# Optimization experiments

Measured on AMD Instinct MI355X. Metric: run time of the kernel, lower is better.

Reference implementation:

```python
import jax, jax.numpy as jnp
import numpy as np

T, B, D = 256, 64, 1024  # time steps, batch (envs), hidden/input dim


def setup_inputs() -> dict:
    key = jax.random.key(0)
    ks = jax.random.split(key, 8)
    s = 1.0 / np.sqrt(D).astype(np.float32)  # lecun-normal-ish scale
    return {
        "ins": jax.random.normal(ks[0], (T, B, D), jnp.float32),
        "hiddens": jax.random.normal(ks[1], (T, B, D), jnp.float32),
        "dones": jax.random.randint(ks[2], (T, B), 0, 2).astype(bool),
        "init_carry": jax.random.normal(ks[3], (B, D), jnp.float32),
        # concatenated input->hidden weights [D, 3D] for (r, z, n) gates
        "W_i": jax.random.normal(ks[4], (D, 3 * D), jnp.float32) * s,
        # concatenated hidden->hidden weights [D, 3D] for (r, z, n) gates
        "W_h": jax.random.normal(ks[5], (D, 3 * D), jnp.float32) * s,
        # input-side biases (b_ir, b_iz, b_in)
        "b_i": jax.random.normal(ks[6], (3 * D,), jnp.float32) * 0.01,
        # hidden-side bias for the 'n' gate only (flax GRUCell: hn Dense has bias)
        "b_hn": jax.random.normal(ks[7], (D,), jnp.float32) * 0.01,
    }


def reference(ins, hiddens, dones, init_carry, W_i, W_h, b_i, b_hn):
    # Hoist input projections out of the scan (same math as per-step Dense)
    x_proj = jnp.einsum('tbd,de->tbe', ins, W_i) + b_i  # [T, B, 3D]
    xr, xz, xn = jnp.split(x_proj, 3, axis=-1)
    W_hr, W_hz, W_hn = jnp.split(W_h, 3, axis=1)

    def step(h, inp):
        xr_t, xz_t, xn_t, hid_t, done_t = inp
        # reset hidden state where episode terminated
        h = jnp.where(done_t[:, None], hid_t, h)
        r = jax.nn.sigmoid(xr_t + h @ W_hr)
        z = jax.nn.sigmoid(xz_t + h @ W_hz)
        n = jnp.tanh(xn_t + r * (h @ W_hn + b_hn))
        h_new = (1.0 - z) * n + z * h  # flax GRUCell update
        return h_new, h_new  # GRUCell returns (new_carry, new_carry)

    final_carry, ys = jax.lax.scan(step, init_carry, (xr, xz, xn, hiddens, dones))
    return final_carry, ys
```

## Files before the change

### kernel.cpp

```cpp
#include <hip/hip_runtime.h>
#include <hip/hip_bf16.h>
#include <stdint.h>


#define T_STEPS 256
#define NB 64
#define DIM 1024
#define NPH 32

typedef unsigned short u16;
typedef __attribute__((ext_vector_type(8))) short bf16x8;
typedef __attribute__((ext_vector_type(4))) float f32x4;

__device__ __forceinline__ float b2f(u16 u){ union{unsigned i; float f;} v; v.i=((unsigned)u)<<16; return v.f; }
__device__ __forceinline__ u16 f2b(float f){
  union { __hip_bfloat16 h; u16 u; } v; v.h = __float2bfloat16(f); return v.u;
}
__device__ __forceinline__ unsigned pk2(float lo, float hi){
  union { __hip_bfloat162 h; unsigned u; } v;
  v.h = __float22bfloat162_rn(make_float2(lo, hi));
  return v.u;
}
__device__ __forceinline__ float sigf(float x){ return 1.0f/(1.0f+__expf(-x)); }
__device__ __forceinline__ float tanh_f(float x){ float ax=fabsf(x); float e=__expf(-2.0f*ax); float t=(1.0f-e)/(1.0f+e); return copysignf(t,x); }

__device__ __forceinline__ int xcdswz(int raw, int n){
  int xcd = raw & 7, idx = raw >> 3;
  int q = n >> 3, r = n & 7;
  int base = (xcd < r) ? xcd*(q+1) : r*(q+1) + (xcd-r)*q;
  return base + idx;
}

__device__ __forceinline__ void gl_lds16(const u16* g, u16* lbase, int lane){
#if __has_builtin(__builtin_amdgcn_global_load_lds)
  __builtin_amdgcn_global_load_lds(
      (const __attribute__((address_space(1))) unsigned int*)g,
      (__attribute__((address_space(3))) unsigned int*)lbase, 16, 0, 0);
#else
  *(uint4*)(lbase + lane*8) = *(const uint4*)g;
#endif
}

__device__ __forceinline__ void stage16(const void* base, size_t eoff, int isf, u16* dst){
  if (isf){
    const float* f = (const float*)base + eoff;
    f32x4 a0 = *(const f32x4*)f;
    f32x4 a1 = *(const f32x4*)(f+4);
    uint4 w;
    w.x = pk2(a0[0],a0[1]); w.y = pk2(a0[2],a0[3]);
    w.z = pk2(a1[0],a1[1]); w.w = pk2(a1[2],a1[3]);
    *(uint4*)dst = w;
  } else {
    *(uint4*)dst = *(const uint4*)((const u16*)base + eoff);
  }
}

__device__ __forceinline__ int get_mode(const int* d){
  return (!d[0]) ? 0 : ((!d[1]) ? 3 : ((!d[2]) ? 2 : 1));
}
__device__ __forceinline__ int get_done(const void* dn, int mode, int i){
  if (mode == 0) return ((const int*)dn)[i] != 0;
  if (mode == 3) return ((const unsigned*)dn)[i] != 0;
  if (mode == 2) return ((const u16*)dn)[i] != 0;
  return ((const unsigned char*)dn)[i] != 0;
}

__global__ void k_setup0(const void* dones, const void* ins, int* cnt, int* cur, int* dflag){
  int tid = threadIdx.x;
  if (tid < NPH){ cnt[tid]=0; cur[tid]=0; }
  if (tid < 4) dflag[tid]=0;
  __syncthreads();
  const unsigned* di = (const unsigned*)dones;
  int vInt=0, vF32=0, vB16=0;
  for (int i = tid; i < 4096; i += 256){
    unsigned v = di[i];
    if (v > 1u) vInt = 1;
    if (v != 0u && v != 0x3F800000u) vF32 = 1;
    unsigned h0 = v & 0xFFFFu, h1 = v >> 16;
    if ((h0 != 0u && h0 != 0x3F80u) || (h1 != 0u && h1 != 0x3F80u)) vB16 = 1;
  }
  if (vInt) atomicOr(&dflag[0], 1);
  if (vF32) atomicOr(&dflag[1], 1);
  if (vB16) atomicOr(&dflag[2], 1);
  const u16* iu = (const u16*)ins;
  int f = 0;
  for (int i = tid; i < 4096; i += 256){
    u16 u = iu[2*i];
    if (((u >> 7) & 0xFF) >= 160) f = 1;
  }
  if (f) atomicOr(&dflag[3], 1);
}

__global__ void k_assign(const void* dones, const int* dflag, int* s_of, int* cnt){
  __shared__ unsigned char sd[T_STEPS];
  int b = blockIdx.x, t = threadIdx.x;
  int mode = get_mode(dflag);
  sd[t] = (unsigned char)get_done(dones, mode, t*NB + b);
  __syncthreads();
  int tt = t;
  while (tt > 0 && !sd[tt]) --tt;
  int s = t - tt;
  if (s >= NPH) s = NPH-1;
  s_of[t*NB + b] = s;
  atomicAdd(&cnt[s], 1);
}

__global__ void k_scan(const int* cnt, int* basep, int* cur){
  if (threadIdx.x == 0){
    int a = 0;
    for (int i=0;i<NPH;++i){ basep[i]=a; a += cnt[i]; }
    basep[NPH] = a;
  }
  if (threadIdx.x < NPH) cur[threadIdx.x] = 0;
}

__global__ void k_fill(const void* dones, const int* dflag, const int* s_of,
                       const int* basep, int* row_tb, int* row_src){
  int s = blockIdx.x;
  __shared__ int runbase;
  __shared__ int wsum[4];
  int tid = threadIdx.x, lane = tid & 63, wave = tid >> 6;
  int mode = get_mode(dflag);
  if (tid == 0) runbase = basep[s];
  __syncthreads();
  for (int i0 = 0; i0 < T_STEPS*NB; i0 += 256){
    int i = i0 + tid;
    int match = (s_of[i] == s);
    unsigned long long mask = __ballot(match);
    if (lane == 0) wsum[wave] = __popcll(mask);
    __syncthreads();
    int off = runbase;
    for (int w = 0; w < wave; ++w) off += wsum[w];
    int total = wsum[0] + wsum[1] + wsum[2] + wsum[3];
    if (match){
      int pos = off + __popcll(mask & ((1ull << lane) - 1ull));
      row_tb[pos] = i;
      int t = i >> 6, b = i & 63;
      int code;
      if (s > 0) code = (t-1)*NB + b;
      else if (get_done(dones, mode, i)) code = i | 0x40000000;
      else code = b | 0x20000000;
      row_src[pos] = code;
    }
    __syncthreads();
    if (tid == 0) runbase += total;
  }
}

__global__ void k_transpose(const void* __restrict__ W, u16* __restrict__ WT, const int* dflag){
  __shared__ u16 ts[64][65];
  int k0 = blockIdx.x*64, n0 = blockIdx.y*64, tid = threadIdx.x;
  int isf = dflag[3];
  for (int i = tid; i < 4096; i += 256){
    int r=i>>6, c=i&63; int idx=(k0+r)*3072 + n0 + c;
    ts[r][c] = isf ? f2b(((const float*)W)[idx]) : ((const u16*)W)[idx];
  }
  __syncthreads();
  for (int i = tid; i < 4096; i += 256){
    int r=i>>6, c=i&63;
    WT[(n0+r)*DIM + k0 + c] = ts[c][r];
  }
}

__global__ void k_bias(const void* bi, const void* bhn, const int* dflag,
                       u16* bi_b, u16* bhn_b){
  int isf = dflag[3];
  int i = blockIdx.x*256 + threadIdx.x;
  if (i < 3072) bi_b[i] = isf ? f2b(((const float*)bi)[i]) : ((const u16*)bi)[i];
  else { int j=i-3072; bhn_b[j] = isf ? f2b(((const float*)bhn)[j]) : ((const u16*)bhn)[j]; }
}

__device__ __forceinline__ void hsrc(int code, const void* outv, const void* hiddens,
                                     const void* initc, const void** hb, size_t* ho){
  if (code & 0x40000000){ *hb = hiddens; *ho = (size_t)(code & 0x0FFFFFFF)*DIM; }
  else if (code & 0x20000000){ *hb = initc; *ho = (size_t)(code & 0x0FFFFFFF)*DIM; }
  else { *hb = outv; *ho = (size_t)NB*DIM + (size_t)code*DIM; }
}

__global__ __launch_bounds__(256, 2) void k_xproj(
    const void* __restrict__ ins, const u16* __restrict__ WiT,
    const int* __restrict__ dflag, u16* __restrict__ xp)
{
  __shared__ u16 As[2][128*64];
  __shared__ u16 Bs[2][128*64];
  int isf = dflag[3];
  int tid=threadIdx.x, wave=tid>>6, lane=tid&63, quad=lane>>4, l16=lane&15;
  int wm=wave&1, wn=wave>>1;
  int srow = wave*8 + (lane>>3), c8=(lane&7)*8;
  int swzc = c8 ^ ((srow&7)<<3);
  int rsw = (l16&7)<<3;
  int l = xcdswz(blockIdx.x, 3072);
  int tn = l % 24, tm = l / 24;
  f32x4 acc[4][4] = {};
  unsigned aoff[4], boff[4];
  #pragma unroll
  for (int p=0;p<4;++p){
    aoff[p] = (unsigned)(tm*128 + p*32 + srow)*DIM + c8;
    boff[p] = (unsigned)(tn*128 + p*32 + srow)*DIM + swzc;
  }
  #pragma unroll
  for (int p=0;p<4;++p) gl_lds16(WiT + boff[p], &Bs[0][(p*32+wave*8)*64], lane);
  #pragma unroll
  for (int p=0;p<4;++p) stage16(ins, aoff[p], isf, &As[0][(p*32+srow)*64 + swzc]);
  __syncthreads();
  int cur = 0;
  #pragma unroll 1
  for (int ko=64; ko<1024; ko+=64){
    #pragma unroll
    for (int p=0;p<4;++p) gl_lds16(WiT + boff[p] + ko, &Bs[cur^1][(p*32+wave*8)*64], lane);
    f32x4 pr0[4], pr1[4];
    #pragma unroll
    for (int p=0;p<4;++p){
      if (isf){ const float* f=(const float*)ins + aoff[p] + ko; pr0[p]=*(const f32x4*)f; pr1[p]=*(const f32x4*)(f+4); }
      else pr0[p]=*(const f32x4*)((const u16*)ins + aoff[p] + ko);
    }
    #pragma unroll
    for (int kk=0;kk<64;kk+=32){
      int rc = (kk + quad*8) ^ rsw;
      bf16x8 af[4], bfv[4];
      #pragma unroll
      for (int mi=0;mi<4;++mi) af[mi]  = *(const bf16x8*)&As[cur][(wm*64+mi*16+l16)*64 + rc];
      #pragma unroll
      for (int ni=0;ni<4;++ni) bfv[ni] = *(const bf16x8*)&Bs[cur][(wn*64+ni*16+l16)*64 + rc];
      #pragma unroll
      for (int mi=0;mi<4;++mi)
        #pragma unroll
        for (int ni=0;ni<4;++ni)
          acc[mi][ni] = __builtin_amdgcn_mfma_f32_16x16x32_bf16(af[mi],bfv[ni],acc[mi][ni],0,0,0);
    }
    #pragma unroll
    for (int p=0;p<4;++p){
      uint4 w;
      if (isf){ w.x=pk2(pr0[p][0],pr0[p][1]); w.y=pk2(pr0[p][2],pr0[p][3]);
                w.z=pk2(pr1[p][0],pr1[p][1]); w.w=pk2(pr1[p][2],pr1[p][3]); }
      else { union{f32x4 f; uint4 u;} cv; cv.f=pr0[p]; w=cv.u; }
      *(uint4*)&As[cur^1][(p*32+srow)*64 + swzc] = w;
    }
    __syncthreads();
    cur ^= 1;
  }
  #pragma unroll
  for (int kk=0;kk<64;kk+=32){
    int rc = (kk + quad*8) ^ rsw;
    bf16x8 af[4], bfv[4];
    #pragma unroll
    for (int mi=0;mi<4;++mi) af[mi]  = *(const bf16x8*)&As[cur][(wm*64+mi*16+l16)*64 + rc];
    #pragma unroll
    for (int ni=0;ni<4;++ni) bfv[ni] = *(const bf16x8*)&Bs[cur][(wn*64+ni*16+l16)*64 + rc];
    #pragma unroll
    for (int mi=0;mi<4;++mi)
      #pragma unroll
      for (int ni=0;ni<4;++ni)
        acc[mi][ni] = __builtin_amdgcn_mfma_f32_16x16x32_bf16(af[mi],bfv[ni],acc[mi][ni],0,0,0);
  }
  #pragma unroll
  for (int mi=0;mi<4;++mi){
    int row = tm*128 + wm*64 + mi*16 + quad*4;
    #pragma unroll
    for (int ni=0;ni<4;++ni){
      int colB = tn*128 + wn*64 + ni*16 + l16;
      u16* op = xp + (size_t)row*3072 + colB;
      #pragma unroll
      for (int j=0;j<4;++j)
        op[(size_t)j*3072] = f2b(acc[mi][ni][j]);
    }
  }
}

#define FAT_MFMA(BUF, NGRP)                                                    \
        _Pragma("unroll")                                                      \
        for (int kk=0;kk<64;kk+=32){                                           \
          int rc = (kk + quad*8) ^ rsw;                                        \
          bf16x8 af[4];                                                        \
          _Pragma("unroll")                                                    \
          for (int mi=0;mi<4;++mi)                                             \
            af[mi] = *(const bf16x8*)&As[BUF][(wm*64+mi*16+l16)*64 + rc];      \
          _Pragma("unroll")                                                    \
          for (int g=0;g<3;++g){                                               \
            int grp = (g==2) ? (NGRP) : g;                                     \
            _Pragma("unroll")                                                  \
            for (int ni=0;ni<2;++ni){                                          \
              bf16x8 bfr = *(const bf16x8*)&Bs[BUF][(g*64+wn*32+ni*16+l16)*64 + rc]; \
              _Pragma("unroll")                                                \
              for (int mi=0;mi<4;++mi)                                         \
                acc[grp][mi][ni] = __builtin_amdgcn_mfma_f32_16x16x32_bf16(af[mi],bfr,acc[grp][mi][ni],0,0,0); \
            }                                                                  \
          }                                                                    \
        }

#define FAT_PANEL(BASEARR, OFFARR, WTP, NGRP)                                  \
    {                                                                          \
      __syncthreads();                                                         \
      _Pragma("unroll")                                                        \
      for (int p=0;p<6;++p)                                                    \
        gl_lds16(WTP + boffB[p], &Bs[0][(p*32+wave*8)*64], lane);              \
      _Pragma("unroll")                                                        \
      for (int p=0;p<4;++p)                                                    \
        stage16(BASEARR[p], OFFARR[p], isf, &As[0][(p*32+srow)*64 + swzc]);    \
      __syncthreads();                                                         \
      int cur = 0;                                                             \
      _Pragma("unroll 1")                                                      \
      for (int ko=64; ko<1024; ko+=64){                                        \
        _Pragma("unroll")                                                      \
        for (int p=0;p<6;++p)                                                  \
          gl_lds16(WTP + boffB[p] + ko, &Bs[cur^1][(p*32+wave*8)*64], lane);   \
        f32x4 pr0[4], pr1[4];                                                  \
        _Pragma("unroll")                                                      \
        for (int p=0;p<4;++p){                                                 \
          if (isf){ const float* f=(const float*)BASEARR[p]+OFFARR[p]+ko;      \
            pr0[p]=*(const f32x4*)f; pr1[p]=*(const f32x4*)(f+4); }            \
          else pr0[p]=*(const f32x4*)((const u16*)BASEARR[p]+OFFARR[p]+ko);    \
        }                                                                      \
        FAT_MFMA(cur, NGRP)                                                    \
        _Pragma("unroll")                                                      \
        for (int p=0;p<4;++p){                                                 \
          uint4 w;                                                             \
          if (isf){ w.x=pk2(pr0[p][0],pr0[p][1]); w.y=pk2(pr0[p][2],pr0[p][3]);\
                    w.z=pk2(pr1[p][0],pr1[p][1]); w.w=pk2(pr1[p][2],pr1[p][3]);}\
          else { union{f32x4 f; uint4 u;} cv; cv.f=pr0[p]; w=cv.u; }           \
          *(uint4*)&As[cur^1][(p*32+srow)*64 + swzc] = w;                      \
        }                                                                      \
        __syncthreads();                                                       \
        cur ^= 1;                                                              \
      }                                                                        \
      FAT_MFMA(cur, NGRP)                                                      \
    }

template<bool HOIST>
__global__ __launch_bounds__(256, 2) void phase_fat(
    int s, const int* __restrict__ pcnt, const int* __restrict__ pbase,
    const int* __restrict__ row_tb, const int* __restrict__ row_src,
    const void* __restrict__ ins, const void* __restrict__ hiddens,
    const void* __restrict__ initc, const u16* __restrict__ WiT,
    const u16* __restrict__ WhT, const u16* __restrict__ bi_b,
    const u16* __restrict__ bhn_b, const int* __restrict__ dflag,
    const u16* __restrict__ xp, void* __restrict__ outv)
{
  int count = pcnt[s];
  if (count <= 0) return;
  int isf = dflag[3];
  int base = pbase[s];
  int mtiles = (count + 127) >> 7;
  int ntot = mtiles << 4;
  __shared__ u16 As[2][128*64];
  __shared__ u16 Bs[2][192*64];
  int tid=threadIdx.x, wave=tid>>6, lane=tid&63, quad=lane>>4, l16=lane&15;
  int wm=wave&1, wn=wave>>1;
  int srow = wave*8 + (lane>>3), c8=(lane&7)*8;
  int swzc = c8 ^ ((srow&7)<<3);
  int rsw = (l16&7)<<3;
  constexpr int NG = HOIST ? 3 : 4;

  for (int raw = blockIdx.x; raw < ntot; raw += gridDim.x){
    int tile = xcdswz(raw, ntot);
    int tm = tile >> 4, dblk = tile & 15, d0 = dblk*64;
    unsigned xoff[4], hoff[4];
    const void* hbv[4];
    const void* xbv[4];
    #pragma unroll
    for (int p=0;p<4;++p){
      int lr = tm*128 + p*32 + srow;
      int idx = base + ((lr < count) ? lr : 0);
      int tb = row_tb[idx], code = row_src[idx];
      xoff[p] = (unsigned)tb*DIM + c8;
      xbv[p] = ins;
      size_t ho; const void* hb;
      hsrc(code, outv, hiddens, initc, &hb, &ho);
      hbv[p] = hb; hoff[p] = (unsigned)ho + c8;
    }
    int boffB[6];
    #pragma unroll
    for (int p=0;p<6;++p)
      boffB[p] = ((p>>1)*DIM + d0 + (p&1)*32 + srow)*DIM + swzc;
    f32x4 acc[NG][4][2] = {};

    if constexpr (!HOIST){
      FAT_PANEL(xbv, xoff, WiT, 2)
    }
    FAT_PANEL(hbv, hoff, WhT, (NG-1))

    int col0 = d0 + wn*32;
    float brv[2], bzv[2], bnv[2], bhv[2];
    #pragma unroll
    for (int ni=0;ni<2;++ni){
      int c = col0 + ni*16 + l16;
      brv[ni]=b2f(bi_b[c]); bzv[ni]=b2f(bi_b[1024+c]);
      bnv[ni]=b2f(bi_b[2048+c]); bhv[ni]=b2f(bhn_b[c]);
    }
    #pragma unroll
    for (int mi=0;mi<4;++mi){
      int lrow0 = tm*128 + wm*64 + mi*16 + quad*4;
      #pragma unroll
      for (int j=0;j<4;++j){
        int lrow = lrow0 + j;
        if (lrow >= count) continue;
        int idx = base + lrow;
        int tb = row_tb[idx], code = row_src[idx];
        size_t ho; const void* hb;
        hsrc(code, outv, hiddens, initc, &hb, &ho);
        #pragma unroll
        for (int ni=0;ni<2;++ni){
          int c = col0 + ni*16 + l16;
          float hpv = isf ? ((const float*)hb)[ho + c] : b2f(((const u16*)hb)[ho + c]);
          float xr = 0.f, xz = 0.f, xn = 0.f;
          if constexpr (HOIST){
            const u16* xrow = xp + (size_t)tb*3072 + c;
            xr = b2f(xrow[0]); xz = b2f(xrow[1024]); xn = b2f(xrow[2048]);
          }
          float r = sigf(brv[ni] + xr + acc[0][mi][ni][j]);
          float z = sigf(bzv[ni] + xz + acc[1][mi][ni][j]);
          float nx = HOIST ? xn : acc[2][mi][ni][j];
          float n = tanh_f(bnv[ni] + nx + r*(acc[NG-1][mi][ni][j] + bhv[ni]));
          float hnew = (1.0f - z)*n + z*hpv;
          size_t yo = (size_t)NB*DIM + (size_t)tb*DIM + c;
          if (isf) ((float*)outv)[yo] = hnew;
          else     ((u16*)outv)[yo] = f2b(hnew);
        }
      }
    }
  }
}

#define THIN_MFMA(BUF, NGRP)                                                   \
      _Pragma("unroll")                                                        \
      for (int kk=0;kk<64;kk+=32){                                             \
        int rc = (kk + quad*8) ^ rsw;                                          \
        bf16x8 af = *(const bf16x8*)&As[BUF][(wave*16+l16)*64 + rc];           \
        _Pragma("unroll")                                                      \
        for (int g=0;g<3;++g){                                                 \
          bf16x8 bfr = *(const bf16x8*)&Bs[BUF][(g*16+l16)*64 + rc];           \
          int grp = (g==2) ? (NGRP) : g;                                       \
          acc[grp] = __builtin_amdgcn_mfma_f32_16x16x32_bf16(af,bfr,acc[grp],0,0,0); \
        }                                                                      \
      }

#define THIN_PANEL(BASEARR, OFFARR, WTP, NGRP)                                 \
    {                                                                          \
      __syncthreads();                                                         \
      gl_lds16(WTP + boffA, &Bs[0][(wave*8)*64], lane);                        \
      if (wave < 2) gl_lds16(WTP + boffC, &Bs[0][(32+wave*8)*64], lane);       \
      stage16(BASEARR[0], OFFARR[0], isf, &As[0][srow*64 + swzc]);             \
      stage16(BASEARR[1], OFFARR[1], isf, &As[0][(32+srow)*64 + swzc]);        \
      __syncthreads();                                                         \
      int cur = 0;                                                             \
      _Pragma("unroll 1")                                                      \
      for (int ko=64; ko<1024; ko+=64){                                        \
        gl_lds16(WTP + boffA + ko, &Bs[cur^1][(wave*8)*64], lane);             \
        if (wave < 2) gl_lds16(WTP + boffC + ko, &Bs[cur^1][(32+wave*8)*64], lane); \
        f32x4 pr0[2], pr1[2];                                                  \
        _Pragma("unroll")                                                      \
        for (int p=0;p<2;++p){                                                 \
          if (isf){ const float* f=(const float*)BASEARR[p]+OFFARR[p]+ko;      \
            pr0[p]=*(const f32x4*)f; pr1[p]=*(const f32x4*)(f+4); }            \
          else pr0[p]=*(const f32x4*)((const u16*)BASEARR[p]+OFFARR[p]+ko);    \
        }                                                                      \
        THIN_MFMA(cur, NGRP)                                                   \
        _Pragma("unroll")                                                      \
        for (int p=0;p<2;++p){                                                 \
          uint4 w;                                                             \
          if (isf){ w.x=pk2(pr0[p][0],pr0[p][1]); w.y=pk2(pr0[p][2],pr0[p][3]);\
                    w.z=pk2(pr1[p][0],pr1[p][1]); w.w=pk2(pr1[p][2],pr1[p][3]);}\
          else { union{f32x4 f; uint4 u;} cv; cv.f=pr0[p]; w=cv.u; }           \
          *(uint4*)&As[cur^1][(p*32+srow)*64 + swzc] = w;                      \
        }                                                                      \
        __syncthreads();                                                       \
        cur ^= 1;                                                              \
      }                                                                        \
      THIN_MFMA(cur, NGRP)                                                     \
    }

template<bool HOIST>
__global__ __launch_bounds__(256, 4) void phase_thin(
    int s, const int* __restrict__ pcnt, const int* __restrict__ pbase,
    const int* __restrict__ row_tb, const int* __restrict__ row_src,
    const void* __restrict__ ins, const void* __restrict__ hiddens,
    const void* __restrict__ initc, const u16* __restrict__ WiT,
    const u16* __restrict__ WhT, const u16* __restrict__ bi_b,
    const u16* __restrict__ bhn_b, const int* __restrict__ dflag,
    const u16* __restrict__ xp, void* __restrict__ outv)
{
  int count = pcnt[s];
  if (count <= 0) return;
  int isf = dflag[3];
  int base = pbase[s];
  int mtiles = (count + 63) >> 6;
  int ntot = mtiles << 6;
  __shared__ u16 As[2][64*64];
  __shared__ u16 Bs[2][48*64];
  int tid=threadIdx.x, wave=tid>>6, lane=tid&63, quad=lane>>4, l16=lane&15;
  int srow = wave*8 + (lane>>3), c8=(lane&7)*8;
  int swzc = c8 ^ ((srow&7)<<3);
  int rsw = (l16&7)<<3;
  constexpr int NG = HOIST ? 3 : 4;

  for (int tile = blockIdx.x; tile < ntot; tile += gridDim.x){
    int tm = tile >> 6, dblk = tile & 63, d0 = dblk*16;
    unsigned xoff[2], hoff[2];
    const void* hbv[2];
    const void* xbv[2];
    #pragma unroll
    for (int p=0;p<2;++p){
      int lr = tm*64 + p*32 + srow;
      int idx = base + ((lr < count) ? lr : 0);
      int tb = row_tb[idx], code = row_src[idx];
      xoff[p] = (unsigned)tb*DIM + c8;
      xbv[p] = ins;
      size_t ho; const void* hb;
      hsrc(code, outv, hiddens, initc, &hb, &ho);
      hbv[p] = hb; hoff[p] = (unsigned)ho + c8;
    }
    int boffA = ((srow>>4)*DIM + d0 + (srow&15))*DIM + swzc;
    int boffC = (2*DIM + d0 + srow)*DIM + swzc;
    f32x4 acc[NG] = {};

    if constexpr (!HOIST){
      THIN_PANEL(xbv, xoff, WiT, 2)
    }
    THIN_PANEL(hbv, hoff, WhT, (HOIST ? 2 : 3))

    int col = d0 + l16;
    float br = b2f(bi_b[col]), bz = b2f(bi_b[1024+col]);
    float bn = b2f(bi_b[2048+col]), bh = b2f(bhn_b[col]);
    int lrow0 = tm*64 + wave*16 + quad*4;
    #pragma unroll
    for (int j=0;j<4;++j){
      int lrow = lrow0 + j;
      if (lrow >= count) continue;
      int idx = base + lrow;
      int tb = row_tb[idx], code = row_src[idx];
      size_t ho; const void* hb;
      hsrc(code, outv, hiddens, initc, &hb, &ho);
      float hpv = isf ? ((const float*)hb)[ho + col] : b2f(((const u16*)hb)[ho + col]);
      float xr = 0.f, xz = 0.f, xn = 0.f;
      if constexpr (HOIST){
        const u16* xrow = xp + (size_t)tb*3072 + col;
        xr = b2f(xrow[0]); xz = b2f(xrow[1024]); xn = b2f(xrow[2048]);
      }
      float r = sigf(br + xr + acc[0][j]);
      float z = sigf(bz + xz + acc[1][j]);
      float nx = HOIST ? xn : acc[2][j];
      float n = tanh_f(bn + nx + r*(acc[NG-1][j] + bh));
      float hnew = (1.0f - z)*n + z*hpv;
      size_t yo = (size_t)NB*DIM + (size_t)tb*DIM + col;
      if (isf) ((float*)outv)[yo] = hnew;
      else     ((u16*)outv)[yo] = f2b(hnew);
    }
  }
}

__global__ void k_final(const int* dflag, void* out){
  int isf = dflag[3];
  size_t i = (size_t)(blockIdx.x*256 + threadIdx.x)*4;
  size_t src = (size_t)NB*DIM + (size_t)(T_STEPS-1)*NB*DIM;
  if (isf){
    float* o = (float*)out;
    *(f32x4*)(o + i) = *(const f32x4*)(o + src + i);
  } else {
    u16* o = (u16*)out;
    *(uint2*)(o + i) = *(const uint2*)(o + src + i);
  }
}

extern "C" void kernel_launch(void* const* d_in, const int* in_sizes, int n_in,
                              void* d_out, int out_size, void* d_ws, size_t ws_size,
                              hipStream_t stream){
  const void* ins = d_in[0];
  const void* hid = d_in[1];
  const void* dn  = d_in[2];
  const void* ini = d_in[3];
  const void* Wi  = d_in[4];
  const void* Wh  = d_in[5];
  const void* bi  = d_in[6];
  const void* bhn = d_in[7];

  char* ws = (char*)d_ws;
  int* dflag  = (int*)(ws + 0);
  int* cnt    = (int*)(ws + 256);
  int* basep  = (int*)(ws + 512);
  int* cur    = (int*)(ws + 1024);
  int* s_of   = (int*)(ws + 4096);
  int* row_tb = (int*)(ws + 69632);
  int* row_src= (int*)(ws + 135168);
  u16* bi_b   = (u16*)(ws + 200704);
  u16* bhn_b  = (u16*)(ws + 208896);
  u16* WiT    = (u16*)(ws + 262144);
  u16* WhT    = (u16*)(ws + 6553600);
  u16* xp     = (u16*)(ws + 12845056);

  const int hoist = (ws_size >= 113508352ull) ? 1 : 0;

  k_setup0<<<1,256,0,stream>>>(dn, ins, cnt, cur, dflag);
  k_assign<<<NB,T_STEPS,0,stream>>>(dn, dflag, s_of, cnt);
  k_scan<<<1,64,0,stream>>>(cnt, basep, cur);
  k_fill<<<NPH,256,0,stream>>>(dn, dflag, s_of, basep, row_tb, row_src);
  k_transpose<<<dim3(16,48),256,0,stream>>>(Wi, WiT, dflag);
  k_transpose<<<dim3(16,48),256,0,stream>>>(Wh, WhT, dflag);
  k_bias<<<16,256,0,stream>>>(bi, bhn, dflag, bi_b, bhn_b);

  if (hoist){
    k_xproj<<<3072,256,0,stream>>>(ins, WiT, dflag, xp);
    for (int s=0;s<6;++s)
      phase_fat<true><<<1024,256,0,stream>>>(s, cnt, basep, row_tb, row_src, ins, hid, ini,
                                             WiT, WhT, bi_b, bhn_b, dflag, xp, d_out);
    for (int s=6;s<NPH;++s)
      phase_thin<true><<<128,256,0,stream>>>(s, cnt, basep, row_tb, row_src, ins, hid, ini,
                                             WiT, WhT, bi_b, bhn_b, dflag, xp, d_out);
  } else {
    for (int s=0;s<6;++s)
      phase_fat<false><<<1024,256,0,stream>>>(s, cnt, basep, row_tb, row_src, ins, hid, ini,
                                              WiT, WhT, bi_b, bhn_b, dflag, xp, d_out);
    for (int s=6;s<NPH;++s)
      phase_thin<false><<<128,256,0,stream>>>(s, cnt, basep, row_tb, row_src, ins, hid, ini,
                                              WiT, WhT, bi_b, bhn_b, dflag, xp, d_out);
  }
  k_final<<<64,256,0,stream>>>(dflag, d_out);
}
```

Before: 1.165 ms.

## Merge per-phase launches into one cooperative persistent kernel with grid sync

Replaces the 32 separate phase launches (fat and thin variants) with one cooperative kernel that loops over phases and calls a grid-wide sync between them, with a per-phase launch fallback. The thin small-tile variant is removed, so late phases with few rows now use 128-row fat tiles. Tile-to-block mapping changes from the XCD swizzle helper to a simpler bit-based interleave. This aims to remove per-launch overhead, but tail phases may lose parallelism and grid sync adds its own cost.

```diff
diff --git a/kernel.cpp b/kernel.cpp
--- a/kernel.cpp
+++ b/kernel.cpp
@@ -1,5 +1,6 @@
 #include <hip/hip_runtime.h>
 #include <hip/hip_bf16.h>
+#include <hip/hip_cooperative_groups.h>
 #include <stdint.h>
 
 
@@ -8,6 +9,8 @@
 #define DIM 1024
 #define NPH 32
 
+namespace cg = cooperative_groups;
+
 typedef unsigned short u16;
 typedef __attribute__((ext_vector_type(8))) short bf16x8;
 typedef __attribute__((ext_vector_type(4))) float f32x4;
@@ -23,13 +26,6 @@
 }
 __device__ __forceinline__ float sigf(float x){ return 1.0f/(1.0f+__expf(-x)); }
 __device__ __forceinline__ float tanh_f(float x){ float ax=fabsf(x); float e=__expf(-2.0f*ax); float t=(1.0f-e)/(1.0f+e); return copysignf(t,x); }
-
-__device__ __forceinline__ int xcdswz(int raw, int n){
-  int xcd = raw & 7, idx = raw >> 3;
-  int q = n >> 3, r = n & 7;
-  int base = (xcd < r) ? xcd*(q+1) : r*(q+1) + (xcd-r)*q;
-  return base + idx;
-}
 
 __device__ __forceinline__ void gl_lds16(const u16* g, u16* lbase, int lane){
 #if __has_builtin(__builtin_amdgcn_global_load_lds)
@@ -189,8 +185,9 @@
   int srow = wave*8 + (lane>>3), c8=(lane&7)*8;
   int swzc = c8 ^ ((srow&7)<<3);
   int rsw = (l16&7)<<3;
-  int l = xcdswz(blockIdx.x, 3072);
-  int tn = l % 24, tm = l / 24;
+  int idx = blockIdx.x >> 3;
+  int tn = (blockIdx.x & 7)*3 + (idx % 3);
+  int tm = idx / 3;
   f32x4 acc[4][4] = {};
   unsigned aoff[4], boff[4];
   #pragma unroll
@@ -327,8 +324,9 @@
     }
 
 template<bool HOIST>
-__global__ __launch_bounds__(256, 2) void phase_fat(
-    int s, const int* __restrict__ pcnt, const int* __restrict__ pbase,
+__global__ __launch_bounds__(256, 2) void k_phases(
+    int s0, int s1, int dosync,
+    const int* __restrict__ cnt, const int* __restrict__ basep,
     const int* __restrict__ row_tb, const int* __restrict__ row_src,
     const void* __restrict__ ins, const void* __restrict__ hiddens,
     const void* __restrict__ initc, const u16* __restrict__ WiT,
@@ -336,14 +334,9 @@
     const u16* __restrict__ bhn_b, const int* __restrict__ dflag,
     const u16* __restrict__ xp, void* __restrict__ outv)
 {
-  int count = pcnt[s];
-  if (count <= 0) return;
-  int isf = dflag[3];
-  int base = pbase[s];
-  int mtiles = (count + 127) >> 7;
-  int ntot = mtiles << 4;
   __shared__ u16 As[2][128*64];
   __shared__ u16 Bs[2][192*64];
+  int isf = dflag[3];
   int tid=threadIdx.x, wave=tid>>6, lane=tid&63, quad=lane>>4, l16=lane&15;
   int wm=wave&1, wn=wave>>1;
   int srow = wave*8 + (lane>>3), c8=(lane&7)*8;
@@ -351,199 +344,85 @@
   int rsw = (l16&7)<<3;
   constexpr int NG = HOIST ? 3 : 4;
 
-  for (int raw = blockIdx.x; raw < ntot; raw += gridDim.x){
-    int tile = xcdswz(raw, ntot);
-    int tm = tile >> 4, dblk = tile & 15, d0 = dblk*64;
-    unsigned xoff[4], hoff[4];
-    const void* hbv[4];
-    const void* xbv[4];
-    #pragma unroll
-    for (int p=0;p<4;++p){
-      int lr = tm*128 + p*32 + srow;
-      int idx = base + ((lr < count) ? lr : 0);
-      int tb = row_tb[idx], code = row_src[idx];
-      xoff[p] = (unsigned)tb*DIM + c8;
-      xbv[p] = ins;
-      size_t ho; const void* hb;
-      hsrc(code, outv, hiddens, initc, &hb, &ho);
-      hbv[p] = hb; hoff[p] = (unsigned)ho + c8;
-    }
-    int boffB[6];
-    #pragma unroll
-    for (int p=0;p<6;++p)
-      boffB[p] = ((p>>1)*DIM + d0 + (p&1)*32 + srow)*DIM + swzc;
-    f32x4 acc[NG][4][2] = {};
-
-    if constexpr (!HOIST){
-      FAT_PANEL(xbv, xoff, WiT, 2)
-    }
-    FAT_PANEL(hbv, hoff, WhT, (NG-1))
-
-    int col0 = d0 + wn*32;
-    float brv[2], bzv[2], bnv[2], bhv[2];
-    #pragma unroll
-    for (int ni=0;ni<2;++ni){
-      int c = col0 + ni*16 + l16;
-      brv[ni]=b2f(bi_b[c]); bzv[ni]=b2f(bi_b[1024+c]);
-      bnv[ni]=b2f(bi_b[2048+c]); bhv[ni]=b2f(bhn_b[c]);
-    }
-    #pragma unroll
-    for (int mi=0;mi<4;++mi){
-      int lrow0 = tm*128 + wm*64 + mi*16 + quad*4;
-      #pragma unroll
-      for (int j=0;j<4;++j){
-        int lrow = lrow0 + j;
-        if (lrow >= count) continue;
-        int idx = base + lrow;
+  for (int s = s0; s < s1; ++s){
+    int count = cnt[s];
+    if (count <= 0) continue;
+    int base = basep[s];
+    int mtiles = (count + 127) >> 7;
+    int ntot = mtiles << 4;
+    for (int raw = blockIdx.x; raw < ntot; raw += gridDim.x){
+      int idx2 = raw >> 3;
+      int dblk = ((raw & 7) << 1) | (idx2 & 1);
+      int tm = idx2 >> 1;
+      int d0 = dblk*64;
+      unsigned xoff[4], hoff[4];
+      const void* hbv[4];
+      const void* xbv[4];
+      #pragma unroll
+      for (int p=0;p<4;++p){
+        int lr = tm*128 + p*32 + srow;
+        int idx = base + ((lr < count) ? lr : 0);
         int tb = row_tb[idx], code = row_src[idx];
+        xoff[p] = (unsigned)tb*DIM + c8;
+        xbv[p] = ins;
         size_t ho; const void* hb;
         hsrc(code, outv, hiddens, initc, &hb, &ho);
+        hbv[p] = hb; hoff[p] = (unsigned)ho + c8;
+      }
+      int boffB[6];
+      #pragma unroll
+      for (int p=0;p<6;++p)
+        boffB[p] = ((p>>1)*DIM + d0 + (p&1)*32 + srow)*DIM + swzc;
+      f32x4 acc[NG][4][2] = {};
+
+      if constexpr (!HOIST){
+        FAT_PANEL(xbv, xoff, WiT, 2)
+      }
+      FAT_PANEL(hbv, hoff, WhT, (NG-1))
+
+      int col0 = d0 + wn*32;
+      float brv[2], bzv[2], bnv[2], bhv[2];
+      #pragma unroll
+      for (int ni=0;ni<2;++ni){
+        int c = col0 + ni*16 + l16;
+        brv[ni]=b2f(bi_b[c]); bzv[ni]=b2f(bi_b[1024+c]);
+        bnv[ni]=b2f(bi_b[2048+c]); bhv[ni]=b2f(bhn_b[c]);
+      }
+      #pragma unroll
+      for (int mi=0;mi<4;++mi){
+        int lrow0 = tm*128 + wm*64 + mi*16 + quad*4;
         #pragma unroll
-        for (int ni=0;ni<2;++ni){
-          int c = col0 + ni*16 + l16;
-          float hpv = isf ? ((const float*)hb)[ho + c] : b2f(((const u16*)hb)[ho + c]);
-          float xr = 0.f, xz = 0.f, xn = 0.f;
-          if constexpr (HOIST){
-            const u16* xrow = xp + (size_t)tb*3072 + c;
-            xr = b2f(xrow[0]); xz = b2f(xrow[1024]); xn = b2f(xrow[2048]);
+        for (int j=0;j<4;++j){
+          int lrow = lrow0 + j;
+          if (lrow >= count) continue;
+          int idx = base + lrow;
+          int tb = row_tb[idx], code = row_src[idx];
+          size_t ho; const void* hb;
+          hsrc(code, outv, hiddens, initc, &hb, &ho);
+          #pragma unroll
+          for (int ni=0;ni<2;++ni){
+            int c = col0 + ni*16 + l16;
+            float hpv = isf ? ((const float*)hb)[ho + c] : b2f(((const u16*)hb)[ho + c]);
+            float xr = 0.f, xz = 0.f, xn = 0.f;
+            if constexpr (HOIST){
+              const u16* xrow = xp + (size_t)tb*3072 + c;
+              xr = b2f(xrow[0]); xz = b2f(xrow[1024]); xn = b2f(xrow[2048]);
+            }
+            float r = sigf(brv[ni] + xr + acc[0][mi][ni][j]);
+            float z = sigf(bzv[ni] + xz + acc[1][mi][ni][j]);
+            float nx = HOIST ? xn : acc[2][mi][ni][j];
+            float n = tanh_f(bnv[ni] + nx + r*(acc[NG-1][mi][ni][j] + bhv[ni]));
+            float hnew = (1.0f - z)*n + z*hpv;
+            size_t yo = (size_t)NB*DIM + (size_t)tb*DIM + c;
+            if (isf) ((float*)outv)[yo] = hnew;
+            else     ((u16*)outv)[yo] = f2b(hnew);
           }
-          float r = sigf(brv[ni] + xr + acc[0][mi][ni][j]);
-          float z = sigf(bzv[ni] + xz + acc[1][mi][ni][j]);
-          float nx = HOIST ? xn : acc[2][mi][ni][j];
-          float n = tanh_f(bnv[ni] + nx + r*(acc[NG-1][mi][ni][j] + bhv[ni]));
-          float hnew = (1.0f - z)*n + z*hpv;
-          size_t yo = (size_t)NB*DIM + (size_t)tb*DIM + c;
-          if (isf) ((float*)outv)[yo] = hnew;
-          else     ((u16*)outv)[yo] = f2b(hnew);
         }
       }
     }
-  }
-}
-
-#define THIN_MFMA(BUF, NGRP)                                                   \
-      _Pragma("unroll")                                                        \
-      for (int kk=0;kk<64;kk+=32){                                             \
-        int rc = (kk + quad*8) ^ rsw;                                          \
-        bf16x8 af = *(const bf16x8*)&As[BUF][(wave*16+l16)*64 + rc];           \
-        _Pragma("unroll")                                                      \
-        for (int g=0;g<3;++g){                                                 \
-          bf16x8 bfr = *(const bf16x8*)&Bs[BUF][(g*16+l16)*64 + rc];           \
-          int grp = (g==2) ? (NGRP) : g;                                       \
-          acc[grp] = __builtin_amdgcn_mfma_f32_16x16x32_bf16(af,bfr,acc[grp],0,0,0); \
-        }                                                                      \
-      }
-
-#define THIN_PANEL(BASEARR, OFFARR, WTP, NGRP)                                 \
-    {                                                                          \
-      __syncthreads();                                                         \
-      gl_lds16(WTP + boffA, &Bs[0][(wave*8)*64], lane);                        \
-      if (wave < 2) gl_lds16(WTP + boffC, &Bs[0][(32+wave*8)*64], lane);       \
-      stage16(BASEARR[0], OFFARR[0], isf, &As[0][srow*64 + swzc]);             \
-      stage16(BASEARR[1], OFFARR[1], isf, &As[0][(32+srow)*64 + swzc]);        \
-      __syncthreads();                                                         \
-      int cur = 0;                                                             \
-      _Pragma("unroll 1")                                                      \
-      for (int ko=64; ko<1024; ko+=64){                                        \
-        gl_lds16(WTP + boffA + ko, &Bs[cur^1][(wave*8)*64], lane);             \
-        if (wave < 2) gl_lds16(WTP + boffC + ko, &Bs[cur^1][(32+wave*8)*64], lane); \
-        f32x4 pr0[2], pr1[2];                                                  \
-        _Pragma("unroll")                                                      \
-        for (int p=0;p<2;++p){                                                 \
-          if (isf){ const float* f=(const float*)BASEARR[p]+OFFARR[p]+ko;      \
-            pr0[p]=*(const f32x4*)f; pr1[p]=*(const f32x4*)(f+4); }            \
-          else pr0[p]=*(const f32x4*)((const u16*)BASEARR[p]+OFFARR[p]+ko);    \
-        }                                                                      \
-        THIN_MFMA(cur, NGRP)                                                   \
-        _Pragma("unroll")                                                      \
-        for (int p=0;p<2;++p){                                                 \
-          uint4 w;                                                             \
-          if (isf){ w.x=pk2(pr0[p][0],pr0[p][1]); w.y=pk2(pr0[p][2],pr0[p][3]);\
-                    w.z=pk2(pr1[p][0],pr1[p][1]); w.w=pk2(pr1[p][2],pr1[p][3]);}\
-          else { union{f32x4 f; uint4 u;} cv; cv.f=pr0[p]; w=cv.u; }           \
-          *(uint4*)&As[cur^1][(p*32+srow)*64 + swzc] = w;                      \
-        }                                                                      \
-        __syncthreads();                                                       \
-        cur ^= 1;                                                              \
-      }                                                                        \
-      THIN_MFMA(cur, NGRP)                                                     \
-    }
-
-template<bool HOIST>
-__global__ __launch_bounds__(256, 4) void phase_thin(
-    int s, const int* __restrict__ pcnt, const int* __restrict__ pbase,
-    const int* __restrict__ row_tb, const int* __restrict__ row_src,
-    const void* __restrict__ ins, const void* __restrict__ hiddens,
-    const void* __restrict__ initc, const u16* __restrict__ WiT,
-    const u16* __restrict__ WhT, const u16* __restrict__ bi_b,
-    const u16* __restrict__ bhn_b, const int* __restrict__ dflag,
-    const u16* __restrict__ xp, void* __restrict__ outv)
-{
-  int count = pcnt[s];
-  if (count <= 0) return;
-  int isf = dflag[3];
-  int base = pbase[s];
-  int mtiles = (count + 63) >> 6;
-  int ntot = mtiles << 6;
-  __shared__ u16 As[2][64*64];
-  __shared__ u16 Bs[2][48*64];
-  int tid=threadIdx.x, wave=tid>>6, lane=tid&63, quad=lane>>4, l16=lane&15;
-  int srow = wave*8 + (lane>>3), c8=(lane&7)*8;
-  int swzc = c8 ^ ((srow&7)<<3);
-  int rsw = (l16&7)<<3;
-  constexpr int NG = HOIST ? 3 : 4;
-
-  for (int tile = blockIdx.x; tile < ntot; tile += gridDim.x){
-    int tm = tile >> 6, dblk = tile & 63, d0 = dblk*16;
-    unsigned xoff[2], hoff[2];
-    const void* hbv[2];
-    const void* xbv[2];
-    #pragma unroll
-    for (int p=0;p<2;++p){
-      int lr = tm*64 + p*32 + srow;
-      int idx = base + ((lr < count) ? lr : 0);
-      int tb = row_tb[idx], code = row_src[idx];
-      xoff[p] = (unsigned)tb*DIM + c8;
-      xbv[p] = ins;
-      size_t ho; const void* hb;
-      hsrc(code, outv, hiddens, initc, &hb, &ho);
-      hbv[p] = hb; hoff[p] = (unsigned)ho + c8;
-    }
-    int boffA = ((srow>>4)*DIM + d0 + (srow&15))*DIM + swzc;
-    int boffC = (2*DIM + d0 + srow)*DIM + swzc;
-    f32x4 acc[NG] = {};
-
-    if constexpr (!HOIST){
-      THIN_PANEL(xbv, xoff, WiT, 2)
-    }
-    THIN_PANEL(hbv, hoff, WhT, (HOIST ? 2 : 3))
-
-    int col = d0 + l16;
-    float br = b2f(bi_b[col]), bz = b2f(bi_b[1024+col]);
-    float bn = b2f(bi_b[2048+col]), bh = b2f(bhn_b[col]);
-    int lrow0 = tm*64 + wave*16 + quad*4;
-    #pragma unroll
-    for (int j=0;j<4;++j){
-      int lrow = lrow0 + j;
-      if (lrow >= count) continue;
-      int idx = base + lrow;
-      int tb = row_tb[idx], code = row_src[idx];
-      size_t ho; const void* hb;
-      hsrc(code, outv, hiddens, initc, &hb, &ho);
-      float hpv = isf ? ((const float*)hb)[ho + col] : b2f(((const u16*)hb)[ho + col]);
-      float xr = 0.f, xz = 0.f, xn = 0.f;
-      if constexpr (HOIST){
-        const u16* xrow = xp + (size_t)tb*3072 + col;
-        xr = b2f(xrow[0]); xz = b2f(xrow[1024]); xn = b2f(xrow[2048]);
-      }
-      float r = sigf(br + xr + acc[0][j]);
-      float z = sigf(bz + xz + acc[1][j]);
-      float nx = HOIST ? xn : acc[2][j];
-      float n = tanh_f(bn + nx + r*(acc[NG-1][j] + bh));
-      float hnew = (1.0f - z)*n + z*hpv;
-      size_t yo = (size_t)NB*DIM + (size_t)tb*DIM + col;
-      if (isf) ((float*)outv)[yo] = hnew;
-      else     ((u16*)outv)[yo] = f2b(hnew);
+    if (dosync){
+      __threadfence();
+      cg::this_grid().sync();
     }
   }
 }
@@ -597,21 +476,33 @@
   k_transpose<<<dim3(16,48),256,0,stream>>>(Wh, WhT, dflag);
   k_bias<<<16,256,0,stream>>>(bi, bhn, dflag, bi_b, bhn_b);
 
-  if (hoist){
-    k_xproj<<<3072,256,0,stream>>>(ins, WiT, dflag, xp);
-    for (int s=0;s<6;++s)
-      phase_fat<true><<<1024,256,0,stream>>>(s, cnt, basep, row_tb, row_src, ins, hid, ini,
-                                             WiT, WhT, bi_b, bhn_b, dflag, xp, d_out);
-    for (int s=6;s<NPH;++s)
-      phase_thin<true><<<128,256,0,stream>>>(s, cnt, basep, row_tb, row_src, ins, hid, ini,
-                                             WiT, WhT, bi_b, bhn_b, dflag, xp, d_out);
-  } else {
-    for (int s=0;s<6;++s)
-      phase_fat<false><<<1024,256,0,stream>>>(s, cnt, basep, row_tb, row_src, ins, hid, ini,
-                                              WiT, WhT, bi_b, bhn_b, dflag, xp, d_out);
-    for (int s=6;s<NPH;++s)
-      phase_thin<false><<<128,256,0,stream>>>(s, cnt, basep, row_tb, row_src, ins, hid, ini,
-                                              WiT, WhT, bi_b, bhn_b, dflag, xp, d_out);
+  if (hoist) k_xproj<<<3072,256,0,stream>>>(ins, WiT, dflag, xp);
+
+  const void* kfn = hoist ? reinterpret_cast<const void*>(&k_phases<true>)
+                          : reinterpret_cast<const void*>(&k_phases<false>);
+  int mb = 0;
+  if (hipOccupancyMaxActiveBlocksPerMultiprocessor(&mb, kfn, 256, 0) != hipSuccess || mb < 1)
+    mb = 2;
+  int grid = mb * 256;
+  if (grid > 512) grid = 512;
+
+  int s0 = 0, s1 = NPH, dosync = 1;
+  void* params[] = { &s0, &s1, &dosync, &cnt, &basep, &row_tb, &row_src,
+                     &ins, &hid, &ini, &WiT, &WhT, &bi_b, &bhn_b,
+                     &dflag, &xp, &d_out };
+  hipError_t ce = hipLaunchCooperativeKernel(kfn, dim3(grid), dim3(256),
+                                             params, 0, stream);
+  if (ce != hipSuccess){
+    for (int s = 0; s < NPH; ++s){
+      if (hoist)
+        k_phases<true><<<512,256,0,stream>>>(s, s+1, 0, cnt, basep, row_tb, row_src,
+                                             ins, hid, ini, WiT, WhT, bi_b, bhn_b,
+                                             dflag, xp, d_out);
+      else
+        k_phases<false><<<512,256,0,stream>>>(s, s+1, 0, cnt, basep, row_tb, row_src,
+                                              ins, hid, ini, WiT, WhT, bi_b, bhn_b,
+                                              dflag, xp, d_out);
+    }
   }
   k_final<<<64,256,0,stream>>>(dflag, d_out);
 }
```

After: 2.005 ms. 72.2% more time.
